# Kernel tuning notes

Measured on AMD Instinct MI355X. Metric: run time of the kernel, lower is better.

Reference implementation:

```python
import jax, jax.numpy as jnp
import numpy as np

MARGIN = 0.3
NUM_CLASSES = 1000


def setup_inputs() -> dict:
    key = jax.random.key(0)
    k1, k2 = jax.random.split(key)
    B, D = 8192, 256
    inputs = jax.random.normal(k1, (B, D), dtype=jnp.float32)
    targets = jax.random.randint(k2, (B,), 0, NUM_CLASSES, dtype=jnp.int64)
    return {"inputs": inputs, "targets": targets}


def reference(inputs, targets):
    # Squared Euclidean pairwise distances: ||x_i||^2 + ||x_j||^2 - 2 x_i.x_j
    sq = jnp.sum(inputs * inputs, axis=1)                      # [B]
    dist = sq[:, None] + sq[None, :] - 2.0 * (inputs @ inputs.T)  # [B, B]

    # Hard mining: per-row max over positives (same label, incl. self),
    # min over negatives, exactly as the torch per-row masked max/min loop.
    pos_mask = targets[:, None] == targets[None, :]            # [B, B] bool
    neg_inf = jnp.float32(-jnp.inf)
    pos_inf = jnp.float32(jnp.inf)
    dist_ap = jnp.max(jnp.where(pos_mask, dist, neg_inf), axis=1)  # [B]
    dist_an = jnp.min(jnp.where(pos_mask, pos_inf, dist), axis=1)  # [B]

    # MarginRankingLoss(margin)(dist_an, dist_ap, y=1) = mean relu(ap - an + m)
    loss = jnp.mean(jax.nn.relu(dist_ap - dist_an + MARGIN))
    prec = jnp.mean((dist_an > dist_ap).astype(jnp.float32))
    return (loss, prec)
```

## Files before the change

kernel.cpp:

```cpp
#include <hip/hip_runtime.h>
#include <hip/hip_bf16.h>

#define B_N 8192
#define D_K 256
#define MARGIN 0.3f

typedef float f32x4 __attribute__((ext_vector_type(4)));
typedef short s16x8 __attribute__((ext_vector_type(8)));

__device__ __forceinline__ unsigned fkey(float f) {
    unsigned u = __float_as_uint(f);
    return (u & 0x80000000u) ? ~u : (u | 0x80000000u);
}
__device__ __forceinline__ float kval(unsigned k) {
    return (k & 0x80000000u) ? __uint_as_float(k ^ 0x80000000u)
                             : __uint_as_float(~k);
}

__device__ __forceinline__ void load_lds16(const unsigned short* g,
                                           unsigned short* l) {
    __builtin_amdgcn_global_load_lds(
        (const __attribute__((address_space(1))) unsigned int*)g,
        (__attribute__((address_space(3))) unsigned int*)l, 16, 0, 0);
}

__global__ __launch_bounds__(256) void prep_kernel(const float* __restrict__ X,
        float* __restrict__ sq, unsigned* __restrict__ apk,
        unsigned* __restrict__ ank, unsigned short* __restrict__ Xp,
        float* __restrict__ acc2) {
    int row  = (blockIdx.x << 2) + (threadIdx.x >> 6);
    int lane = threadIdx.x & 63;
    const float4 v = reinterpret_cast<const float4*>(X + (size_t)row * D_K)[lane];

    float xs[4] = {v.x, v.y, v.z, v.w};
    ushort4 hv;
    unsigned short* hp = &hv.x;
    float s = 0.f;
    #pragma unroll
    for (int i = 0; i < 4; ++i) {
        __hip_bfloat16 h = __float2bfloat16(xs[i]);
        hp[i] = *reinterpret_cast<unsigned short*>(&h);
        float hf = __bfloat162float(h);
        s = fmaf(hf, hf, s);
    }
    *reinterpret_cast<ushort4*>(Xp + (size_t)row * D_K + lane * 4) = hv;

    #pragma unroll
    for (int o = 32; o > 0; o >>= 1) s += __shfl_down(s, o, 64);
    if (lane == 0) {
        sq[row]  = s;
        apk[row] = 0u;
        ank[row] = 0xFFFFFFFFu;
    }
    if (blockIdx.x == 0 && threadIdx.x == 0) {
        acc2[0] = 0.f; acc2[1] = 0.f;
        reinterpret_cast<unsigned*>(acc2)[2] = 0u;
    }
}

#define BM 128
#define BN 128

__global__ __launch_bounds__(256, 4) void dist_kernel(
        const unsigned short* __restrict__ Xp,
        const int* __restrict__ tgt, const float* __restrict__ sq,
        unsigned* __restrict__ apk, unsigned* __restrict__ ank) {
    __shared__ unsigned short Atile[128 * 64];
    __shared__ unsigned short Btile[128 * 64];

    const int t    = threadIdx.x;
    const int lane = t & 63;
    const int wave = t >> 6;
    const int wrow = (wave >> 1) * 64;
    const int wcol = (wave & 1) * 64;
    const int fr   = lane & 15;
    const int quad = lane >> 4;
    const float INF = __int_as_float(0x7f800000);

    int tt = blockIdx.x;
    int bx = (int)((sqrtf(8.f * (float)tt + 1.f) - 1.f) * 0.5f);
    while ((bx + 1) * (bx + 2) / 2 <= tt) ++bx;
    while (bx * (bx + 1) / 2 > tt) --bx;
    int by = tt - bx * (bx + 1) / 2;
    const int bm = by * BM;
    const int bn = bx * BN;

    const unsigned short* ag[4];
    const unsigned short* bg[4];
    unsigned short* al[4];
    unsigned short* bl[4];
    #pragma unroll
    for (int j = 0; j < 4; ++j) {
        int g = wave * 64 + j * 256 + lane;
        int r = g >> 3, s0 = g & 7;
        int u = s0 ^ (r & 7);
        ag[j] = Xp + (size_t)(bm + r) * D_K + u * 8;
        bg[j] = Xp + (size_t)(bn + r) * D_K + u * 8;
        al[j] = Atile + g * 8;
        bl[j] = Btile + g * 8;
    }

    f32x4 acc[4][4];
    #pragma unroll
    for (int i = 0; i < 4; ++i)
        #pragma unroll
        for (int j = 0; j < 4; ++j) acc[i][j] = (f32x4){0.f, 0.f, 0.f, 0.f};

    #pragma unroll 1
    for (int win = 0; win < 4; ++win) {
        __syncthreads();
        const int wo = win * 64;
        #pragma unroll
        for (int j = 0; j < 4; ++j) {
            load_lds16(ag[j] + wo, al[j]);
            load_lds16(bg[j] + wo, bl[j]);
        }
        __syncthreads();

        s16x8 a[4][2], b[4][2];
        #pragma unroll
        for (int mi = 0; mi < 4; ++mi) {
            int rb = (wrow + mi * 16 + fr) * 64;
            #pragma unroll
            for (int h = 0; h < 2; ++h) {
                int s = (h * 4 + quad) ^ (fr & 7);
                a[mi][h] = *reinterpret_cast<const s16x8*>(&Atile[rb + s * 8]);
            }
        }
        #pragma unroll
        for (int ni = 0; ni < 4; ++ni) {
            int rb = (wcol + ni * 16 + fr) * 64;
            #pragma unroll
            for (int h = 0; h < 2; ++h) {
                int s = (h * 4 + quad) ^ (fr & 7);
                b[ni][h] = *reinterpret_cast<const s16x8*>(&Btile[rb + s * 8]);
            }
        }
        #pragma unroll
        for (int mi = 0; mi < 4; ++mi)
            #pragma unroll
            for (int ni = 0; ni < 4; ++ni) {
                acc[mi][ni] = __builtin_amdgcn_mfma_f32_16x16x32_bf16(
                    a[mi][0], b[ni][0], acc[mi][ni], 0, 0, 0);
                acc[mi][ni] = __builtin_amdgcn_mfma_f32_16x16x32_bf16(
                    a[mi][1], b[ni][1], acc[mi][ni], 0, 0, 0);
            }
    }

    int   ct[4]; float csq[4];
    #pragma unroll
    for (int ni = 0; ni < 4; ++ni) {
        int c = bn + wcol + ni * 16 + fr;
        ct[ni] = tgt[c]; csq[ni] = sq[c];
    }
    float cap[4], can[4];
    #pragma unroll
    for (int ni = 0; ni < 4; ++ni) { cap[ni] = -INF; can[ni] = INF; }

    #pragma unroll
    for (int mi = 0; mi < 4; ++mi) {
        #pragma unroll
        for (int reg = 0; reg < 4; ++reg) {
            int rl = wrow + mi * 16 + quad * 4 + reg;
            int rt = tgt[bm + rl]; float rsq = sq[bm + rl];
            float rap = -INF, ran = INF;
            #pragma unroll
            for (int ni = 0; ni < 4; ++ni) {
                float d = rsq + csq[ni] - 2.f * acc[mi][ni][reg];
                bool pos = (rt == ct[ni]);
                if (pos) { rap = fmaxf(rap, d); cap[ni] = fmaxf(cap[ni], d); }
                else     { ran = fminf(ran, d); can[ni] = fminf(can[ni], d); }
            }
            #pragma unroll
            for (int o = 1; o < 16; o <<= 1) {
                rap = fmaxf(rap, __shfl_xor(rap, o, 64));
                ran = fminf(ran, __shfl_xor(ran, o, 64));
            }
            if (fr == 0) {
                atomicMax(&apk[bm + rl], fkey(rap));
                atomicMin(&ank[bm + rl], fkey(ran));
            }
        }
    }
    #pragma unroll
    for (int ni = 0; ni < 4; ++ni) {
        #pragma unroll
        for (int o = 16; o < 64; o <<= 1) {
            cap[ni] = fmaxf(cap[ni], __shfl_xor(cap[ni], o, 64));
            can[ni] = fminf(can[ni], __shfl_xor(can[ni], o, 64));
        }
    }
    if (lane < 16) {
        #pragma unroll
        for (int ni = 0; ni < 4; ++ni) {
            int c = bn + wcol + ni * 16 + lane;
            atomicMax(&apk[c], fkey(cap[ni]));
            atomicMin(&ank[c], fkey(can[ni]));
        }
    }
}

__global__ __launch_bounds__(256) void final_kernel(const unsigned* __restrict__ apk,
        const unsigned* __restrict__ ank, float* __restrict__ acc2,
        float* __restrict__ out) {
    __shared__ float s_sum[4], s_cnt[4];
    int i = blockIdx.x * 256 + threadIdx.x;
    float ap = kval(apk[i]);
    float an = kval(ank[i]);
    float v  = ap - an + MARGIN;
    float sum = v > 0.f ? v : 0.f;
    float cnt = an > ap ? 1.f : 0.f;
    #pragma unroll
    for (int o = 32; o > 0; o >>= 1) {
        sum += __shfl_down(sum, o, 64);
        cnt += __shfl_down(cnt, o, 64);
    }
    int wave = threadIdx.x >> 6, lane = threadIdx.x & 63;
    if (lane == 0) { s_sum[wave] = sum; s_cnt[wave] = cnt; }
    __syncthreads();
    if (threadIdx.x == 0) {
        float ts = 0.f, tc = 0.f;
        #pragma unroll
        for (int w = 0; w < 4; ++w) { ts += s_sum[w]; tc += s_cnt[w]; }
        atomicAdd(&acc2[0], ts);
        atomicAdd(&acc2[1], tc);
        __threadfence();
        unsigned ticket = atomicAdd(reinterpret_cast<unsigned*>(acc2) + 2, 1u);
        if (ticket == gridDim.x - 1) {
            float fs = atomicAdd(&acc2[0], 0.f);
            float fc = atomicAdd(&acc2[1], 0.f);
            out[0] = fs / (float)B_N;
            out[1] = fc / (float)B_N;
        }
    }
}

extern "C" void kernel_launch(void* const* d_in, const int* in_sizes, int n_in,
                              void* d_out, int out_size, void* d_ws, size_t ws_size,
                              hipStream_t stream) {
    const float* X   = (const float*)d_in[0];
    const int*   tgt = (const int*)d_in[1];

    char* ws = (char*)d_ws;
    float*          sq   = (float*)ws;
    unsigned*       apk  = (unsigned*)(ws + 32768);
    unsigned*       ank  = (unsigned*)(ws + 65536);
    float*          acc2 = (float*)(ws + 98304);
    unsigned short* Xp   = (unsigned short*)(ws + 131072);

    float* out = (float*)d_out;

    prep_kernel<<<B_N / 4, 256, 0, stream>>>(X, sq, apk, ank, Xp, acc2);
    dist_kernel<<<(64 * 65) / 2, 256, 0, stream>>>(Xp, tgt, sq, apk, ank);
    final_kernel<<<B_N / 256, 256, 0, stream>>>(apk, ank, acc2, out);
}
```

Before: 118.3 us.

## Double-buffer LDS tiles with narrower K windows to overlap loads and MFMA

Splits the K dimension into eight 32-wide windows and ping-pongs two LDS buffers per operand. The next window is prefetched with global_load_lds while the current one feeds the MFMAs, so there is one barrier per window instead of two. The swizzle is rewritten for 32-element rows, and total LDS per block is halved. In exchange there are more loop iterations and barriers, and correctness relies on the barrier waiting for the outstanding async LDS loads.

```diff
diff --git a/kernel.cpp b/kernel.cpp
--- a/kernel.cpp
+++ b/kernel.cpp
@@ -60,13 +60,14 @@
 
 #define BM 128
 #define BN 128
+#define NWIN 8
 
 __global__ __launch_bounds__(256, 4) void dist_kernel(
         const unsigned short* __restrict__ Xp,
         const int* __restrict__ tgt, const float* __restrict__ sq,
         unsigned* __restrict__ apk, unsigned* __restrict__ ank) {
-    __shared__ unsigned short Atile[128 * 64];
-    __shared__ unsigned short Btile[128 * 64];
+    __shared__ unsigned short Atile[2][128 * 32];
+    __shared__ unsigned short Btile[2][128 * 32];
 
     const int t    = threadIdx.x;
     const int lane = t & 63;
@@ -85,19 +86,26 @@
     const int bm = by * BM;
     const int bn = bx * BN;
 
-    const unsigned short* ag[4];
-    const unsigned short* bg[4];
-    unsigned short* al[4];
-    unsigned short* bl[4];
-    #pragma unroll
-    for (int j = 0; j < 4; ++j) {
-        int g = wave * 64 + j * 256 + lane;
-        int r = g >> 3, s0 = g & 7;
-        int u = s0 ^ (r & 7);
+    const unsigned short* ag[2];
+    const unsigned short* bg[2];
+    int loff[2];
+    #pragma unroll
+    for (int j = 0; j < 2; ++j) {
+        int g = j * 256 + t;
+        int r = g >> 2, s0 = g & 3;
+        int u = s0 ^ (r & 3) ^ ((r >> 2) & 3);
         ag[j] = Xp + (size_t)(bm + r) * D_K + u * 8;
         bg[j] = Xp + (size_t)(bn + r) * D_K + u * 8;
-        al[j] = Atile + g * 8;
-        bl[j] = Btile + g * 8;
+        loff[j] = g * 8;
+    }
+
+    const int fswz = (fr & 3) ^ ((fr >> 2) & 3);
+    int aoff[4], boff[4];
+    #pragma unroll
+    for (int i = 0; i < 4; ++i) {
+        int s = quad ^ fswz;
+        aoff[i] = (wrow + i * 16 + fr) * 32 + s * 8;
+        boff[i] = (wcol + i * 16 + fr) * 32 + s * 8;
     }
 
     f32x4 acc[4][4];
@@ -106,45 +114,38 @@
         #pragma unroll
         for (int j = 0; j < 4; ++j) acc[i][j] = (f32x4){0.f, 0.f, 0.f, 0.f};
 
-    #pragma unroll 1
-    for (int win = 0; win < 4; ++win) {
+    #pragma unroll
+    for (int j = 0; j < 2; ++j) {
+        load_lds16(ag[j], &Atile[0][loff[j]]);
+        load_lds16(bg[j], &Btile[0][loff[j]]);
+    }
+
+    #pragma unroll
+    for (int win = 0; win < NWIN; ++win) {
         __syncthreads();
-        const int wo = win * 64;
-        #pragma unroll
-        for (int j = 0; j < 4; ++j) {
-            load_lds16(ag[j] + wo, al[j]);
-            load_lds16(bg[j] + wo, bl[j]);
-        }
-        __syncthreads();
-
-        s16x8 a[4][2], b[4][2];
-        #pragma unroll
-        for (int mi = 0; mi < 4; ++mi) {
-            int rb = (wrow + mi * 16 + fr) * 64;
-            #pragma unroll
-            for (int h = 0; h < 2; ++h) {
-                int s = (h * 4 + quad) ^ (fr & 7);
-                a[mi][h] = *reinterpret_cast<const s16x8*>(&Atile[rb + s * 8]);
-            }
-        }
-        #pragma unroll
-        for (int ni = 0; ni < 4; ++ni) {
-            int rb = (wcol + ni * 16 + fr) * 64;
-            #pragma unroll
-            for (int h = 0; h < 2; ++h) {
-                int s = (h * 4 + quad) ^ (fr & 7);
-                b[ni][h] = *reinterpret_cast<const s16x8*>(&Btile[rb + s * 8]);
-            }
-        }
+        if (win < NWIN - 1) {
+            const int wo = (win + 1) * 32;
+            const int nb = (win + 1) & 1;
+            #pragma unroll
+            for (int j = 0; j < 2; ++j) {
+                load_lds16(ag[j] + wo, &Atile[nb][loff[j]]);
+                load_lds16(bg[j] + wo, &Btile[nb][loff[j]]);
+            }
+        }
+        const int cur = win & 1;
+        s16x8 a[4], b[4];
         #pragma unroll
         for (int mi = 0; mi < 4; ++mi)
-            #pragma unroll
-            for (int ni = 0; ni < 4; ++ni) {
+            a[mi] = *reinterpret_cast<const s16x8*>(&Atile[cur][aoff[mi]]);
+        #pragma unroll
+        for (int ni = 0; ni < 4; ++ni)
+            b[ni] = *reinterpret_cast<const s16x8*>(&Btile[cur][boff[ni]]);
+        #pragma unroll
+        for (int mi = 0; mi < 4; ++mi)
+            #pragma unroll
+            for (int ni = 0; ni < 4; ++ni)
                 acc[mi][ni] = __builtin_amdgcn_mfma_f32_16x16x32_bf16(
-                    a[mi][0], b[ni][0], acc[mi][ni], 0, 0, 0);
-                acc[mi][ni] = __builtin_amdgcn_mfma_f32_16x16x32_bf16(
-                    a[mi][1], b[ni][1], acc[mi][ni], 0, 0, 0);
-            }
+                    a[mi], b[ni], acc[mi][ni], 0, 0, 0);
     }
 
     int   ct[4]; float csq[4];
```

Measured after the change: 123.9 us. 4.8% more time.

## Replace global atomic max/min with per-panel partial buffers reduced in final kernel

Applied to the files above, without the earlier changes.

The distance kernel no longer does global atomicMax/atomicMin on keyed floats. Each block first combines row and column reductions across its two waves in shared memory, then writes them to a per-panel partial array indexed by block row or column. The final kernel reduces the 64 panel partials per row. This removes atomic contention and the init writes, but adds 4 MB of partial traffic, an extra block barrier, and a 64-step strided read loop in the small final kernel.

```diff
diff --git a/kernel.cpp b/kernel.cpp
--- a/kernel.cpp
+++ b/kernel.cpp
@@ -4,18 +4,10 @@
 #define B_N 8192
 #define D_K 256
 #define MARGIN 0.3f
+#define NPAN 64
 
 typedef float f32x4 __attribute__((ext_vector_type(4)));
 typedef short s16x8 __attribute__((ext_vector_type(8)));
-
-__device__ __forceinline__ unsigned fkey(float f) {
-    unsigned u = __float_as_uint(f);
-    return (u & 0x80000000u) ? ~u : (u | 0x80000000u);
-}
-__device__ __forceinline__ float kval(unsigned k) {
-    return (k & 0x80000000u) ? __uint_as_float(k ^ 0x80000000u)
-                             : __uint_as_float(~k);
-}
 
 __device__ __forceinline__ void load_lds16(const unsigned short* g,
                                            unsigned short* l) {
@@ -25,8 +17,7 @@
 }
 
 __global__ __launch_bounds__(256) void prep_kernel(const float* __restrict__ X,
-        float* __restrict__ sq, unsigned* __restrict__ apk,
-        unsigned* __restrict__ ank, unsigned short* __restrict__ Xp,
+        float* __restrict__ sq, unsigned short* __restrict__ Xp,
         float* __restrict__ acc2) {
     int row  = (blockIdx.x << 2) + (threadIdx.x >> 6);
     int lane = threadIdx.x & 63;
@@ -47,11 +38,7 @@
 
     #pragma unroll
     for (int o = 32; o > 0; o >>= 1) s += __shfl_down(s, o, 64);
-    if (lane == 0) {
-        sq[row]  = s;
-        apk[row] = 0u;
-        ank[row] = 0xFFFFFFFFu;
-    }
+    if (lane == 0) sq[row] = s;
     if (blockIdx.x == 0 && threadIdx.x == 0) {
         acc2[0] = 0.f; acc2[1] = 0.f;
         reinterpret_cast<unsigned*>(acc2)[2] = 0u;
@@ -64,9 +51,10 @@
 __global__ __launch_bounds__(256, 4) void dist_kernel(
         const unsigned short* __restrict__ Xp,
         const int* __restrict__ tgt, const float* __restrict__ sq,
-        unsigned* __restrict__ apk, unsigned* __restrict__ ank) {
+        float* __restrict__ part_ap, float* __restrict__ part_an) {
     __shared__ unsigned short Atile[128 * 64];
     __shared__ unsigned short Btile[128 * 64];
+    __shared__ float rowap[128], rowan[128], colap[128], colan[128];
 
     const int t    = threadIdx.x;
     const int lane = t & 63;
@@ -157,6 +145,7 @@
     #pragma unroll
     for (int ni = 0; ni < 4; ++ni) { cap[ni] = -INF; can[ni] = INF; }
 
+    float rapv[16], ranv[16];
     #pragma unroll
     for (int mi = 0; mi < 4; ++mi) {
         #pragma unroll
@@ -176,12 +165,14 @@
                 rap = fmaxf(rap, __shfl_xor(rap, o, 64));
                 ran = fminf(ran, __shfl_xor(ran, o, 64));
             }
-            if (fr == 0) {
-                atomicMax(&apk[bm + rl], fkey(rap));
-                atomicMin(&ank[bm + rl], fkey(ran));
-            }
-        }
-    }
+            rapv[mi * 4 + reg] = rap;
+            ranv[mi * 4 + reg] = ran;
+            if ((wave & 1) == 0 && fr == 0) {
+                rowap[rl] = rap; rowan[rl] = ran;
+            }
+        }
+    }
+
     #pragma unroll
     for (int ni = 0; ni < 4; ++ni) {
         #pragma unroll
@@ -190,23 +181,52 @@
             can[ni] = fminf(can[ni], __shfl_xor(can[ni], o, 64));
         }
     }
-    if (lane < 16) {
+    if (wave < 2 && lane < 16) {
         #pragma unroll
         for (int ni = 0; ni < 4; ++ni) {
-            int c = bn + wcol + ni * 16 + lane;
-            atomicMax(&apk[c], fkey(cap[ni]));
-            atomicMin(&ank[c], fkey(can[ni]));
-        }
-    }
-}
-
-__global__ __launch_bounds__(256) void final_kernel(const unsigned* __restrict__ apk,
-        const unsigned* __restrict__ ank, float* __restrict__ acc2,
-        float* __restrict__ out) {
+            int c = wcol + ni * 16 + lane;
+            colap[c] = cap[ni]; colan[c] = can[ni];
+        }
+    }
+
+    __syncthreads();
+
+    if (wave & 1) {
+        #pragma unroll
+        for (int mi = 0; mi < 4; ++mi)
+            #pragma unroll
+            for (int reg = 0; reg < 4; ++reg) {
+                int rl = wrow + mi * 16 + quad * 4 + reg;
+                if (fr == 0) {
+                    part_ap[(size_t)bx * B_N + bm + rl] =
+                        fmaxf(rapv[mi * 4 + reg], rowap[rl]);
+                    part_an[(size_t)bx * B_N + bm + rl] =
+                        fminf(ranv[mi * 4 + reg], rowan[rl]);
+                }
+            }
+    }
+    if (wave >= 2 && bx != by && lane < 16) {
+        #pragma unroll
+        for (int ni = 0; ni < 4; ++ni) {
+            int c = wcol + ni * 16 + lane;
+            part_ap[(size_t)by * B_N + bn + c] = fmaxf(cap[ni], colap[c]);
+            part_an[(size_t)by * B_N + bn + c] = fminf(can[ni], colan[c]);
+        }
+    }
+}
+
+__global__ __launch_bounds__(256) void final_kernel(
+        const float* __restrict__ part_ap, const float* __restrict__ part_an,
+        float* __restrict__ acc2, float* __restrict__ out) {
     __shared__ float s_sum[4], s_cnt[4];
     int i = blockIdx.x * 256 + threadIdx.x;
-    float ap = kval(apk[i]);
-    float an = kval(ank[i]);
+    float ap = part_ap[i];
+    float an = part_an[i];
+    #pragma unroll 4
+    for (int q = 1; q < NPAN; ++q) {
+        ap = fmaxf(ap, part_ap[(size_t)q * B_N + i]);
+        an = fminf(an, part_an[(size_t)q * B_N + i]);
+    }
     float v  = ap - an + MARGIN;
     float sum = v > 0.f ? v : 0.f;
     float cnt = an > ap ? 1.f : 0.f;
@@ -242,15 +262,15 @@
     const int*   tgt = (const int*)d_in[1];
 
     char* ws = (char*)d_ws;
-    float*          sq   = (float*)ws;
-    unsigned*       apk  = (unsigned*)(ws + 32768);
-    unsigned*       ank  = (unsigned*)(ws + 65536);
-    float*          acc2 = (float*)(ws + 98304);
-    unsigned short* Xp   = (unsigned short*)(ws + 131072);
+    float*          sq      = (float*)ws;
+    float*          acc2    = (float*)(ws + 32768);
+    float*          part_ap = (float*)(ws + 65536);
+    float*          part_an = (float*)(ws + 65536 + 2097152);
+    unsigned short* Xp      = (unsigned short*)(ws + 65536 + 4194304);
 
     float* out = (float*)d_out;
 
-    prep_kernel<<<B_N / 4, 256, 0, stream>>>(X, sq, apk, ank, Xp, acc2);
-    dist_kernel<<<(64 * 65) / 2, 256, 0, stream>>>(Xp, tgt, sq, apk, ank);
-    final_kernel<<<B_N / 256, 256, 0, stream>>>(apk, ank, acc2, out);
-}
+    prep_kernel<<<B_N / 4, 256, 0, stream>>>(X, sq, Xp, acc2);
+    dist_kernel<<<(64 * 65) / 2, 256, 0, stream>>>(Xp, tgt, sq, part_ap, part_an);
+    final_kernel<<<B_N / 256, 256, 0, stream>>>(part_ap, part_an, acc2, out);
+}
```

Result: slower. 120.9 us (+2.2%).
